# Optimization experiments

Measured on AMD Instinct MI355X. Metric: run time of the kernel, lower is better.

## Reference

```python
import jax, jax.numpy as jnp
import numpy as np

N, E, F_IN = 10000, 160000, 256
H1, C1 = 8, 128          # conv1: heads=8, out 128 per head, concat -> 1024
H2, C2 = 1, 64           # conv2: heads=1, out 64
NEG_SLOPE = 0.2


def setup_inputs() -> dict:
    key = jax.random.key(0)
    ks = jax.random.split(key, 10)
    s_in = 1.0 / np.sqrt(F_IN)
    s_h1 = 1.0 / np.sqrt(H1 * C1)
    return {
        "x": jax.random.normal(ks[0], (N, F_IN), dtype=jnp.float32),
        "edge_index": jax.random.randint(ks[1], (2, E), 0, N, dtype=jnp.int64),
        "W1": jax.random.normal(ks[2], (F_IN, H1 * C1), dtype=jnp.float32) * s_in,
        "att_src1": jax.random.normal(ks[3], (H1, C1), dtype=jnp.float32) * 0.1,
        "att_dst1": jax.random.normal(ks[4], (H1, C1), dtype=jnp.float32) * 0.1,
        "b1": jnp.zeros((H1 * C1,), dtype=jnp.float32),
        "W2": jax.random.normal(ks[5], (H1 * C1, H2 * C2), dtype=jnp.float32) * s_h1,
        "att_src2": jax.random.normal(ks[6], (H2, C2), dtype=jnp.float32) * 0.1,
        "att_dst2": jax.random.normal(ks[7], (H2, C2), dtype=jnp.float32) * 0.1,
        "b2": jnp.zeros((H2 * C2,), dtype=jnp.float32),
    }


def gat_conv(x, src, dst, W, att_src, att_dst, b, n):
    """PyG GATConv (eval mode: dropout off), concat=True, add_self_loops handled by caller."""
    H, C = att_src.shape
    h = (x @ W).reshape(n, H, C)                       # [N,H,C]
    a_s = jnp.einsum('nhc,hc->nh', h, att_src)         # [N,H]
    a_d = jnp.einsum('nhc,hc->nh', h, att_dst)         # [N,H]
    e = jax.nn.leaky_relu(a_s[src] + a_d[dst], NEG_SLOPE)  # [Etot,H]
    # softmax over edges grouped by destination node (numerically stable)
    e_max = jax.ops.segment_max(e, dst, num_segments=n)
    e = jnp.exp(e - e_max[dst])
    denom = jax.ops.segment_sum(e, dst, num_segments=n)
    alpha = e / (denom[dst] + 1e-16)                   # [Etot,H]
    msg = h[src] * alpha[:, :, None]                   # [Etot,H,C]
    out = jax.ops.segment_sum(msg, dst, num_segments=n)  # [N,H,C]
    return out.reshape(n, H * C) + b


def reference(x, edge_index, W1, att_src1, att_dst1, b1, W2, att_src2, att_dst2, b2):
    n = x.shape[0]
    loops = jnp.arange(n, dtype=edge_index.dtype)
    src = jnp.concatenate([edge_index[0], loops])
    dst = jnp.concatenate([edge_index[1], loops])
    h = jax.nn.elu(gat_conv(x, src, dst, W1, att_src1, att_dst1, b1, n))
    return gat_conv(h, src, dst, W2, att_src2, att_dst2, b2, n)
```

## Files before the change

kernel.cpp:

```cpp
#include <hip/hip_runtime.h>
#include <cmath>


typedef short bf16x8 __attribute__((ext_vector_type(8)));
typedef float f32x4 __attribute__((ext_vector_type(4)));
typedef unsigned short u16x8 __attribute__((ext_vector_type(8)));

__device__ __forceinline__ float lrelu(float x) { return x > 0.f ? x : 0.2f * x; }
__device__ __forceinline__ float b2f(unsigned short h) {
  return __uint_as_float(((unsigned)h) << 16);
}
__device__ __forceinline__ unsigned short f2bf(float f) {
  unsigned u = __float_as_uint(f);
  u += 0x7FFFu + ((u >> 16) & 1u);
  return (unsigned short)(u >> 16);
}

__device__ __forceinline__ void fma8(float* acc, uint4 v, float e) {
  acc[0] += e * __uint_as_float(v.x << 16);
  acc[1] += e * __uint_as_float(v.x & 0xffff0000u);
  acc[2] += e * __uint_as_float(v.y << 16);
  acc[3] += e * __uint_as_float(v.y & 0xffff0000u);
  acc[4] += e * __uint_as_float(v.z << 16);
  acc[5] += e * __uint_as_float(v.z & 0xffff0000u);
  acc[6] += e * __uint_as_float(v.w << 16);
  acc[7] += e * __uint_as_float(v.w & 0xffff0000u);
}

#define GLOAD_LDS16(gsrc, ldst)                                              \
  __builtin_amdgcn_global_load_lds(                                          \
      (const __attribute__((address_space(1))) unsigned int*)(gsrc),         \
      (__attribute__((address_space(3))) unsigned int*)(ldst), 16, 0, 0)


__global__ __launch_bounds__(256) void prep_fused(
    const int* __restrict__ ei, int* __restrict__ counts, int E,
    const float* __restrict__ x, unsigned short* __restrict__ xpk, int N, int MB1,
    const float* __restrict__ W1, unsigned short* __restrict__ w1pk,
    const float* __restrict__ W2, unsigned short* __restrict__ w2pk) {
  const int countB = (E + 255) / 256;
  const int pxB = MB1 * 8;
  int bid = blockIdx.x;
  int t = threadIdx.x;

  if (bid < countB) {
    int e = bid * 256 + t;
    if (e < E) atomicAdd(&counts[ei[E + e]], 1);
    return;
  }
  bid -= countB;
  if (bid < pxB) {
    int mb = bid >> 3, ks = bid & 7;
    int l = t & 63, f = t >> 6;
    int row = mb * 64 + f * 16 + (l & 15);
    int kc = ks * 32 + (l >> 4) * 8;
    float v[8];
#pragma unroll
    for (int j = 0; j < 8; ++j) v[j] = 0.f;
    if (row < N) {
      const float* xr = x + (size_t)row * 256 + kc;
#pragma unroll
      for (int j = 0; j < 8; ++j) v[j] = xr[j];
    }
    u16x8 hi, lo;
#pragma unroll
    for (int j = 0; j < 8; ++j) {
      unsigned short h = f2bf(v[j]);
      hi[j] = h; lo[j] = f2bf(v[j] - b2f(h));
    }
    size_t base = (size_t)(mb * 8 + ks) * 8 * 512;
    *(u16x8*)(xpk + base + (size_t)f * 512 + l * 8) = hi;
    *(u16x8*)(xpk + base + (size_t)(4 + f) * 512 + l * 8) = lo;
    return;
  }
  bid -= pxB;
  if (bid < 64) {
    int hb = bid >> 3, ks = bid & 7;
    int l = t & 63, gq = t >> 6;
    for (int g = gq; g < 8; g += 4) {
      int n = hb * 128 + g * 16 + (l & 15);
      int k0 = ks * 32 + (l >> 4) * 8;
      u16x8 hi, lo;
#pragma unroll
      for (int j = 0; j < 8; ++j) {
        float v = W1[(size_t)(k0 + j) * 1024 + n];
        unsigned short h = f2bf(v);
        hi[j] = h; lo[j] = f2bf(v - b2f(h));
      }
      size_t base = (size_t)(hb * 8 + ks) * 16 * 512;
      *(u16x8*)(w1pk + base + (size_t)g * 512 + l * 8) = hi;
      *(u16x8*)(w1pk + base + (size_t)(8 + g) * 512 + l * 8) = lo;
    }
    return;
  }
  bid -= 64;
  {
    int ks = bid;
    int l = t & 63, g = t >> 6;
    int n = g * 16 + (l & 15);
    int k0 = ks * 32 + (l >> 4) * 8;
    u16x8 hi, lo;
#pragma unroll
    for (int j = 0; j < 8; ++j) {
      float v = W2[(size_t)(k0 + j) * 64 + n];
      unsigned short h = f2bf(v);
      hi[j] = h; lo[j] = f2bf(v - b2f(h));
    }
    size_t base = (size_t)ks * 8 * 512;
    *(u16x8*)(w2pk + base + (size_t)g * 512 + l * 8) = hi;
    *(u16x8*)(w2pk + base + (size_t)(4 + g) * 512 + l * 8) = lo;
  }
}


__global__ __launch_bounds__(256) void scan_blk(const int* __restrict__ counts,
                                                int* __restrict__ offsets,
                                                int* __restrict__ bsum, int n) {
  __shared__ int lds[256];
  int b = blockIdx.x, t = threadIdx.x, i = b * 256 + t;
  int v = (i < n) ? counts[i] + 1 : 0;
  lds[t] = v;
  __syncthreads();
  for (int off = 1; off < 256; off <<= 1) {
    int tv = (t >= off) ? lds[t - off] : 0;
    __syncthreads();
    lds[t] += tv;
    __syncthreads();
  }
  if (i < n) offsets[i] = lds[t] - v;
  if (t == 255) bsum[b] = lds[255];
}

__global__ __launch_bounds__(256) void scan_apply(int* __restrict__ offsets,
                                                  int* __restrict__ cursors,
                                                  const int* __restrict__ bsum,
                                                  int nb, int n) {
  __shared__ int pre_s;
  int b = blockIdx.x, t = threadIdx.x;
  if (t == 0) {
    int s = 0;
    for (int i = 0; i < b; ++i) s += bsum[i];
    pre_s = s;
    if (b == nb - 1) {
      int tot = s;
      for (int i = b; i < nb; ++i) tot += bsum[i];
      offsets[n] = tot;
    }
  }
  __syncthreads();
  int i = b * 256 + t;
  if (i < n) {
    int o = offsets[i] + pre_s;
    offsets[i] = o;
    cursors[i] = o;
  }
}

__global__ __launch_bounds__(256) void fill_all(const int* __restrict__ ei,
                                                int* __restrict__ cursors,
                                                const int* __restrict__ offsets,
                                                int* __restrict__ list,
                                                int E, int n) {
  int tid = blockIdx.x * 256 + threadIdx.x;
  if (tid < E) {
    int d = ei[E + tid];
    int pos = atomicAdd(&cursors[d], 1);
    list[pos] = ei[tid];
  } else if (tid < E + n) {
    int i = tid - E;
    list[offsets[i + 1] - 1] = i;
  }
}


__global__ __launch_bounds__(512, 4) void gemm1_att(
    const unsigned short* __restrict__ xpk, const unsigned short* __restrict__ w1pk,
    const float* __restrict__ asrc, const float* __restrict__ adst,
    unsigned short* __restrict__ h1b, float* __restrict__ as1,
    float* __restrict__ ad1) {
  extern __shared__ char sm[];
  const int t = threadIdx.x, wid = t >> 6, lane = t & 63;
  const int wr = wid >> 2, wc = wid & 3;
  const int mb = blockIdx.x, hb = blockIdx.y;
  const int m0 = mb * 128;
  const int l15 = lane & 15, l4 = lane >> 4;

  f32x4 acc[4][2] = {};

  auto stage = [&](int buf, int ks) {
    char* base0 = sm + buf * 32768;
    for (int i = wid; i < 32; i += 8) {
      const unsigned short* src;
      int ldsoff;
      if (i < 8) {
        int r = i >> 2;
        src = xpk + (size_t)((2 * mb + r) * 8 + ks) * 4096 + (i & 3) * 512 + lane * 8;
        ldsoff = i * 1024;
      } else if (i < 16) {
        int f = i - 8, r = f >> 2;
        src = xpk + (size_t)((2 * mb + r) * 8 + ks) * 4096 + (4 + (f & 3)) * 512 + lane * 8;
        ldsoff = 8192 + f * 1024;
      } else if (i < 24) {
        int g = i - 16;
        src = w1pk + (size_t)(hb * 8 + ks) * 8192 + g * 512 + lane * 8;
        ldsoff = 16384 + g * 1024;
      } else {
        int g = i - 24;
        src = w1pk + (size_t)(hb * 8 + ks) * 8192 + (8 + g) * 512 + lane * 8;
        ldsoff = 24576 + g * 1024;
      }
      GLOAD_LDS16(src, base0 + ldsoff);
    }
  };

  stage(0, 0);
  __syncthreads();
  int buf = 0;
  for (int step = 0; step < 8; ++step) {
    if (step < 7) stage(buf ^ 1, step + 1);
    const char* b = sm + buf * 32768;
    bf16x8 ah[4], al[4], bh[2], bl[2];
#pragma unroll
    for (int mf = 0; mf < 4; ++mf) {
      ah[mf] = *(const bf16x8*)(b + (wr * 4 + mf) * 1024 + lane * 16);
      al[mf] = *(const bf16x8*)(b + 8192 + (wr * 4 + mf) * 1024 + lane * 16);
    }
#pragma unroll
    for (int nf = 0; nf < 2; ++nf) {
      bh[nf] = *(const bf16x8*)(b + 16384 + (wc * 2 + nf) * 1024 + lane * 16);
      bl[nf] = *(const bf16x8*)(b + 24576 + (wc * 2 + nf) * 1024 + lane * 16);
    }
#pragma unroll
    for (int mf = 0; mf < 4; ++mf)
#pragma unroll
      for (int nf = 0; nf < 2; ++nf) {
        acc[mf][nf] = __builtin_amdgcn_mfma_f32_16x16x32_bf16(ah[mf], bh[nf], acc[mf][nf], 0, 0, 0);
        acc[mf][nf] = __builtin_amdgcn_mfma_f32_16x16x32_bf16(ah[mf], bl[nf], acc[mf][nf], 0, 0, 0);
        acc[mf][nf] = __builtin_amdgcn_mfma_f32_16x16x32_bf16(al[mf], bh[nf], acc[mf][nf], 0, 0, 0);
      }
    __syncthreads();
    buf ^= 1;
  }

  float* parts_s = (float*)sm;
  float* parts_d = (float*)(sm + 2048);
  unsigned short* ctile = (unsigned short*)(sm + 4096);
  float as_c[2], ad_c[2];
#pragma unroll
  for (int nf = 0; nf < 2; ++nf) {
    int col = hb * 128 + wc * 32 + nf * 16 + l15;
    as_c[nf] = asrc[col];
    ad_c[nf] = adst[col];
  }
#pragma unroll
  for (int mf = 0; mf < 4; ++mf) {
    float ss[4] = {0.f, 0.f, 0.f, 0.f}, dd[4] = {0.f, 0.f, 0.f, 0.f};
#pragma unroll
    for (int nf = 0; nf < 2; ++nf)
#pragma unroll
      for (int r = 0; r < 4; ++r) {
        ss[r] += acc[mf][nf][r] * as_c[nf];
        dd[r] += acc[mf][nf][r] * ad_c[nf];
      }
#pragma unroll
    for (int r = 0; r < 4; ++r)
      for (int m = 1; m < 16; m <<= 1) {
        ss[r] += __shfl_xor(ss[r], m);
        dd[r] += __shfl_xor(dd[r], m);
      }
    if (l15 == 0) {
#pragma unroll
      for (int r = 0; r < 4; ++r) {
        int row = wr * 64 + mf * 16 + l4 * 4 + r;
        parts_s[row * 4 + wc] = ss[r];
        parts_d[row * 4 + wc] = dd[r];
      }
    }
#pragma unroll
    for (int nf = 0; nf < 2; ++nf)
#pragma unroll
      for (int r = 0; r < 4; ++r) {
        int row = wr * 64 + mf * 16 + l4 * 4 + r;
        int col = wc * 32 + nf * 16 + l15;
        ctile[row * 128 + col] = f2bf(acc[mf][nf][r]);
      }
  }
  __syncthreads();
  if (t < 128) {
    float s = parts_s[t * 4] + parts_s[t * 4 + 1] + parts_s[t * 4 + 2] + parts_s[t * 4 + 3];
    float d = parts_d[t * 4] + parts_d[t * 4 + 1] + parts_d[t * 4 + 2] + parts_d[t * 4 + 3];
    as1[(size_t)(m0 + t) * 8 + hb] = s;
    ad1[(size_t)(m0 + t) * 8 + hb] = d;
  }
#pragma unroll
  for (int rep = 0; rep < 4; ++rep) {
    int e = rep * 4096 + t * 8;
    int row = e >> 7, col = e & 127;
    bf16x8 v = *(const bf16x8*)(ctile + e);
    *(bf16x8*)(h1b + (size_t)(m0 + row) * 1024 + hb * 128 + col) = v;
  }
}


__global__ __launch_bounds__(256) void agg1_gather(
    const unsigned short* __restrict__ h1b, const float* __restrict__ as1,
    const float* __restrict__ ad1, const int* __restrict__ offsets,
    const int* __restrict__ list, const float* __restrict__ b1,
    unsigned short* __restrict__ o1pk, int n) {
  __shared__ __align__(16) unsigned short stg[8192];
  const int t = threadIdx.x, w = t >> 6, lane = t & 63;
  const int node = blockIdx.x * 4 + w;
  const int h0 = lane >> 4, h1_ = h0 + 4;

  if (node < n) {
    const int beg = offsets[node], end = offsets[node + 1];
    const float ad0 = ad1[(size_t)node * 8 + h0];
    const float ad4 = ad1[(size_t)node * 8 + h1_];
    float acc0[8] = {}, acc1[8] = {};
    float den0 = 0.f, den4 = 0.f;

    int j = beg;
    int sA = 0, sB = 0;
    float aA0 = 0.f, aA4 = 0.f, aB0 = 0.f, aB4 = 0.f;
    uint4 vA0, vA1, vB0, vB1;
    if (j + 2 <= end) {
      sA = list[j]; sB = list[j + 1];
      aA0 = as1[(size_t)sA * 8 + h0]; aA4 = as1[(size_t)sA * 8 + h1_];
      aB0 = as1[(size_t)sB * 8 + h0]; aB4 = as1[(size_t)sB * 8 + h1_];
      vA0 = *(const uint4*)(h1b + (size_t)sA * 1024 + lane * 8);
      vA1 = *(const uint4*)(h1b + (size_t)sA * 1024 + 512 + lane * 8);
      vB0 = *(const uint4*)(h1b + (size_t)sB * 1024 + lane * 8);
      vB1 = *(const uint4*)(h1b + (size_t)sB * 1024 + 512 + lane * 8);
    }
    for (; j + 4 <= end; j += 2) {
      int sA2 = list[j + 2], sB2 = list[j + 3];
      float aA02 = as1[(size_t)sA2 * 8 + h0], aA42 = as1[(size_t)sA2 * 8 + h1_];
      float aB02 = as1[(size_t)sB2 * 8 + h0], aB42 = as1[(size_t)sB2 * 8 + h1_];
      uint4 nA0 = *(const uint4*)(h1b + (size_t)sA2 * 1024 + lane * 8);
      uint4 nA1 = *(const uint4*)(h1b + (size_t)sA2 * 1024 + 512 + lane * 8);
      uint4 nB0 = *(const uint4*)(h1b + (size_t)sB2 * 1024 + lane * 8);
      uint4 nB1 = *(const uint4*)(h1b + (size_t)sB2 * 1024 + 512 + lane * 8);
      float eA0 = __expf(lrelu(aA0 + ad0)), eA4 = __expf(lrelu(aA4 + ad4));
      float eB0 = __expf(lrelu(aB0 + ad0)), eB4 = __expf(lrelu(aB4 + ad4));
      den0 += eA0 + eB0; den4 += eA4 + eB4;
      fma8(acc0, vA0, eA0); fma8(acc1, vA1, eA4);
      fma8(acc0, vB0, eB0); fma8(acc1, vB1, eB4);
      sA = sA2; sB = sB2;
      aA0 = aA02; aA4 = aA42; aB0 = aB02; aB4 = aB42;
      vA0 = nA0; vA1 = nA1; vB0 = nB0; vB1 = nB1;
    }
    if (j + 2 <= end) {
      float eA0 = __expf(lrelu(aA0 + ad0)), eA4 = __expf(lrelu(aA4 + ad4));
      float eB0 = __expf(lrelu(aB0 + ad0)), eB4 = __expf(lrelu(aB4 + ad4));
      den0 += eA0 + eB0; den4 += eA4 + eB4;
      fma8(acc0, vA0, eA0); fma8(acc1, vA1, eA4);
      fma8(acc0, vB0, eB0); fma8(acc1, vB1, eB4);
      j += 2;
    }
    if (j < end) {
      int s = list[j];
      float a0 = as1[(size_t)s * 8 + h0], a4 = as1[(size_t)s * 8 + h1_];
      uint4 v0 = *(const uint4*)(h1b + (size_t)s * 1024 + lane * 8);
      uint4 v1 = *(const uint4*)(h1b + (size_t)s * 1024 + 512 + lane * 8);
      float e0 = __expf(lrelu(a0 + ad0)), e4 = __expf(lrelu(a4 + ad4));
      den0 += e0; den4 += e4;
      fma8(acc0, v0, e0); fma8(acc1, v1, e4);
    }

    const float inv0 = 1.f / (den0 + 1e-16f);
    const float inv4 = 1.f / (den4 + 1e-16f);
    u16x8 hiA, loA, hiB, loB;
#pragma unroll
    for (int k = 0; k < 8; ++k) {
      float vA = acc0[k] * inv0 + b1[lane * 8 + k];
      float vB = acc1[k] * inv4 + b1[512 + lane * 8 + k];
      vA = vA > 0.f ? vA : expm1f(vA);
      vB = vB > 0.f ? vB : expm1f(vB);
      unsigned short hA = f2bf(vA), hB = f2bf(vB);
      hiA[k] = hA; loA[k] = f2bf(vA - b2f(hA));
      hiB[k] = hB; loB[k] = f2bf(vB - b2f(hB));
    }
    const int q2 = lane >> 2, kc = lane & 3;
    {
      int aw = q2 * 512 + kc * 64 + w * 16;
      *(u16x8*)((char*)stg + (aw ^ ((q2 & 7) << 4))) = hiA;
      aw += 256;
      *(u16x8*)((char*)stg + (aw ^ ((q2 & 7) << 4))) = loA;
    }
    {
      int ks = 16 + q2;
      int aw = ks * 512 + kc * 64 + w * 16;
      *(u16x8*)((char*)stg + (aw ^ ((ks & 7) << 4))) = hiB;
      aw += 256;
      *(u16x8*)((char*)stg + (aw ^ ((ks & 7) << 4))) = loB;
    }
  }
  __syncthreads();
  const int blk = blockIdx.x;
  const int mb = blk >> 4, f = (blk >> 2) & 3, l15b = (blk & 3) * 4;
#pragma unroll
  for (int it = 0; it < 4; ++it) {
    int a = it * 4096 + t * 16;
    int ks = a >> 9, half = (a >> 8) & 1, kcc = (a >> 6) & 3, ww = (a >> 4) & 3;
    u16x8 v = *(const u16x8*)((const char*)stg + (a ^ ((ks & 7) << 4)));
    size_t g = (size_t)(mb * 32 + ks) * 4096 + half * 2048 + (size_t)f * 512 +
               (size_t)(kcc * 16 + l15b + ww) * 8;
    *(u16x8*)(o1pk + g) = v;
  }
}


__global__ __launch_bounds__(256) void gemm2_splitk(
    const unsigned short* __restrict__ o1pk, const unsigned short* __restrict__ w2pk,
    float* __restrict__ h2p, int Mpad) {
  extern __shared__ char sm[];
  const int t = threadIdx.x, wid = t >> 6, lane = t & 63;
  const int wr = wid >> 1, wc = wid & 1;
  const int mb = blockIdx.x, sk = blockIdx.y;
  const int m0 = mb * 64;
  const int l15 = lane & 15, l4 = lane >> 4;

  f32x4 acc[2][2] = {};

  auto stage = [&](int buf, int ks) {
    char* base0 = sm + buf * 16384;
    const unsigned short* ax = o1pk + (size_t)(mb * 32 + ks) * 8 * 512 + lane * 8;
    for (int i = wid; i < 8; i += 4)
      GLOAD_LDS16(ax + i * 512, base0 + i * 1024);
    const unsigned short* bw = w2pk + (size_t)ks * 8 * 512 + lane * 8;
    for (int i = wid; i < 8; i += 4)
      GLOAD_LDS16(bw + i * 512, base0 + 8192 + i * 1024);
  };

  stage(0, sk * 8);
  __syncthreads();
  int buf = 0;
  for (int step = 0; step < 8; ++step) {
    if (step < 7) stage(buf ^ 1, sk * 8 + step + 1);
    const char* b = sm + buf * 16384;
    bf16x8 ah[2], al[2], bh[2], bl[2];
#pragma unroll
    for (int mf = 0; mf < 2; ++mf) {
      int f = wr * 2 + mf;
      ah[mf] = *(const bf16x8*)(b + f * 1024 + lane * 16);
      al[mf] = *(const bf16x8*)(b + 4096 + f * 1024 + lane * 16);
    }
#pragma unroll
    for (int nf = 0; nf < 2; ++nf) {
      int g = wc * 2 + nf;
      bh[nf] = *(const bf16x8*)(b + 8192 + g * 1024 + lane * 16);
      bl[nf] = *(const bf16x8*)(b + 12288 + g * 1024 + lane * 16);
    }
#pragma unroll
    for (int mf = 0; mf < 2; ++mf)
#pragma unroll
      for (int nf = 0; nf < 2; ++nf) {
        acc[mf][nf] = __builtin_amdgcn_mfma_f32_16x16x32_bf16(ah[mf], bh[nf], acc[mf][nf], 0, 0, 0);
        acc[mf][nf] = __builtin_amdgcn_mfma_f32_16x16x32_bf16(ah[mf], bl[nf], acc[mf][nf], 0, 0, 0);
        acc[mf][nf] = __builtin_amdgcn_mfma_f32_16x16x32_bf16(al[mf], bh[nf], acc[mf][nf], 0, 0, 0);
      }
    __syncthreads();
    buf ^= 1;
  }

#pragma unroll
  for (int mf = 0; mf < 2; ++mf)
#pragma unroll
    for (int nf = 0; nf < 2; ++nf)
#pragma unroll
      for (int r = 0; r < 4; ++r) {
        int row = wr * 32 + mf * 16 + l4 * 4 + r;
        int col = wc * 32 + nf * 16 + l15;
        h2p[((size_t)sk * Mpad + m0 + row) * 64 + col] = acc[mf][nf][r];
      }
}


__global__ __launch_bounds__(256) void reduce_att2(
    const float* __restrict__ h2p, const float* __restrict__ asrc,
    const float* __restrict__ adst, float* __restrict__ h2,
    float* __restrict__ as2, float* __restrict__ ad2, int Mpad, int n) {
  int w = threadIdx.x >> 6, lane = threadIdx.x & 63;
  int row = blockIdx.x * 4 + w;
  if (row >= n) return;
  float s = 0.f;
#pragma unroll
  for (int sk = 0; sk < 4; ++sk) s += h2p[((size_t)sk * Mpad + row) * 64 + lane];
  h2[(size_t)row * 64 + lane] = s;
  float ds = s * asrc[lane], dd = s * adst[lane];
  for (int o = 32; o; o >>= 1) { ds += __shfl_xor(ds, o); dd += __shfl_xor(dd, o); }
  if (lane == 0) { as2[row] = ds; ad2[row] = dd; }
}


__global__ __launch_bounds__(256) void agg2_gather(
    const float* __restrict__ h2, const float* __restrict__ as2,
    const float* __restrict__ ad2, const int* __restrict__ offsets,
    const int* __restrict__ list, const float* __restrict__ b2,
    float* __restrict__ out, int n) {
  const int wid = threadIdx.x >> 6, lane = threadIdx.x & 63;
  const int node = blockIdx.x * 4 + wid;
  if (node >= n) return;
  const int beg = offsets[node], end = offsets[node + 1];
  const float ad = ad2[node];
  const int cb = (lane & 15) * 4;
  const int jo = lane >> 4;

  float4 acc = make_float4(0.f, 0.f, 0.f, 0.f);
  float den = 0.f;
  for (int j = beg + jo; j < end; j += 4) {
    int s = list[j];
    float e = __expf(lrelu(as2[s] + ad));
    den += e;
    float4 v = *(const float4*)&h2[(size_t)s * 64 + cb];
    acc.x += e * v.x; acc.y += e * v.y; acc.z += e * v.z; acc.w += e * v.w;
  }
  acc.x += __shfl_xor(acc.x, 16); acc.y += __shfl_xor(acc.y, 16);
  acc.z += __shfl_xor(acc.z, 16); acc.w += __shfl_xor(acc.w, 16);
  den += __shfl_xor(den, 16);
  acc.x += __shfl_xor(acc.x, 32); acc.y += __shfl_xor(acc.y, 32);
  acc.z += __shfl_xor(acc.z, 32); acc.w += __shfl_xor(acc.w, 32);
  den += __shfl_xor(den, 32);
  if (jo == 0) {
    float inv = 1.f / (den + 1e-16f);
    float4 r;
    r.x = acc.x * inv + b2[cb];
    r.y = acc.y * inv + b2[cb + 1];
    r.z = acc.z * inv + b2[cb + 2];
    r.w = acc.w * inv + b2[cb + 3];
    *(float4*)&out[(size_t)node * 64 + cb] = r;
  }
}


extern "C" void kernel_launch(void* const* d_in, const int* in_sizes, int n_in,
                              void* d_out, int out_size, void* d_ws, size_t ws_size,
                              hipStream_t stream) {
  const float* x     = (const float*)d_in[0];
  const int*   ei    = (const int*)d_in[1];
  const float* W1    = (const float*)d_in[2];
  const float* asrc1 = (const float*)d_in[3];
  const float* adst1 = (const float*)d_in[4];
  const float* b1    = (const float*)d_in[5];
  const float* W2    = (const float*)d_in[6];
  const float* asrc2 = (const float*)d_in[7];
  const float* adst2 = (const float*)d_in[8];
  const float* b2    = (const float*)d_in[9];
  float* out = (float*)d_out;

  const int N = in_sizes[0] / 256;
  const int E = in_sizes[1] / 2;
  const int T = E + N;
  const int MBB = (N + 127) / 128;
  const int Mpad = MBB * 128;
  const int MB1 = Mpad / 64;
  const int NB = (N + 255) / 256;

  char* p = (char*)d_ws;
  auto bump = [&](size_t bytes) {
    char* r = p;
    p += (bytes + 255) & ~(size_t)255;
    return r;
  };
  int* counts  = (int*)bump((size_t)N * 4);
  int* offsets = (int*)bump((size_t)(N + 1) * 4);
  int* cursors = (int*)bump((size_t)N * 4);
  int* bsum    = (int*)bump((size_t)NB * 4);
  int* list    = (int*)bump((size_t)T * 4);
  unsigned short* xpk  = (unsigned short*)bump((size_t)Mpad * 512 * 2);
  unsigned short* w1pk = (unsigned short*)bump((size_t)8 * 8 * 16 * 512 * 2);
  unsigned short* h1b  = (unsigned short*)bump((size_t)Mpad * 1024 * 2);
  float* as1           = (float*)bump((size_t)Mpad * 8 * 4);
  float* ad1           = (float*)bump((size_t)Mpad * 8 * 4);
  unsigned short* o1pk = (unsigned short*)bump((size_t)Mpad * 2048 * 2);
  unsigned short* w2pk = (unsigned short*)bump((size_t)32 * 8 * 512 * 2);
  float* as2           = (float*)bump((size_t)Mpad * 4);
  float* ad2           = (float*)bump((size_t)Mpad * 4);
  float* h2p = (float*)h1b;
  float* h2  = (float*)xpk;

  hipMemsetAsync(counts, 0, (size_t)N * 4, stream);
  {
    int gridsz = (E + 255) / 256 + MB1 * 8 + 64 + 32;
    prep_fused<<<gridsz, 256, 0, stream>>>(ei, counts, E, x, xpk, N, MB1,
                                           W1, w1pk, W2, w2pk);
  }
  scan_blk<<<NB, 256, 0, stream>>>(counts, offsets, bsum, N);
  scan_apply<<<NB, 256, 0, stream>>>(offsets, cursors, bsum, NB, N);
  fill_all<<<(E + N + 255) / 256, 256, 0, stream>>>(ei, cursors, offsets, list, E, N);

  gemm1_att<<<dim3(MBB, 8), 512, 65536, stream>>>(xpk, w1pk, asrc1, adst1, h1b, as1, ad1);
  agg1_gather<<<(N + 3) / 4, 256, 0, stream>>>(h1b, as1, ad1, offsets, list, b1, o1pk, N);

  gemm2_splitk<<<dim3(Mpad / 64, 4), 256, 32768, stream>>>(o1pk, w2pk, h2p, Mpad);
  reduce_att2<<<(N + 3) / 4, 256, 0, stream>>>(h2p, asrc2, adst2, h2, as2, ad2, Mpad, N);
  agg2_gather<<<(N + 3) / 4, 256, 0, stream>>>(h2, as2, ad2, offsets, list, b2, out, N);
}
```

Before: 162.3 us.

## Drop x low-bf16 split in GEMM1, shrink tiles, and order gather blocks by degree

Removes the low-order bf16 part of x, so GEMM1 runs two MFMAs per fragment pair instead of three and the packed-x buffer is half the size. GEMM1 moves to 64-row tiles with 256 threads and less LDS. Adds three small kernels that bucket 4-node gather blocks by total in-degree, sort them heaviest first, and remap blockIdx in agg1/agg2 through that order to reduce tail imbalance. This lowers GEMM1 accuracy, since x is now effectively rounded to bf16, and adds extra launches plus a memset.

```diff
diff --git a/kernel.cpp b/kernel.cpp
--- a/kernel.cpp
+++ b/kernel.cpp
@@ -62,15 +62,11 @@
 #pragma unroll
       for (int j = 0; j < 8; ++j) v[j] = xr[j];
     }
-    u16x8 hi, lo;
-#pragma unroll
-    for (int j = 0; j < 8; ++j) {
-      unsigned short h = f2bf(v[j]);
-      hi[j] = h; lo[j] = f2bf(v[j] - b2f(h));
-    }
-    size_t base = (size_t)(mb * 8 + ks) * 8 * 512;
+    u16x8 hi;
+#pragma unroll
+    for (int j = 0; j < 8; ++j) hi[j] = f2bf(v[j]);
+    size_t base = (size_t)(mb * 8 + ks) * 4 * 512;
     *(u16x8*)(xpk + base + (size_t)f * 512 + l * 8) = hi;
-    *(u16x8*)(xpk + base + (size_t)(4 + f) * 512 + l * 8) = lo;
     return;
   }
   bid -= pxB;
@@ -173,43 +169,74 @@
 }
 
 
-__global__ __launch_bounds__(512, 4) void gemm1_att(
+__global__ __launch_bounds__(256) void bweight(const int* __restrict__ offsets,
+                                               int* __restrict__ bwgt,
+                                               int* __restrict__ bhist,
+                                               int nblk, int n) {
+  int b = blockIdx.x * 256 + threadIdx.x;
+  if (b >= nblk) return;
+  int lo = b * 4, hi = min(lo + 4, n);
+  int w = min(offsets[hi] - offsets[lo], 1023);
+  bwgt[b] = w;
+  atomicAdd(&bhist[w], 1);
+}
+
+__global__ __launch_bounds__(1024) void bscan(const int* __restrict__ bhist,
+                                              int* __restrict__ doff) {
+  __shared__ int lds[1024];
+  int t = threadIdx.x;
+  lds[t] = bhist[t];
+  __syncthreads();
+  for (int off = 1; off < 1024; off <<= 1) {
+    int v = (t >= off) ? lds[t - off] : 0;
+    __syncthreads();
+    lds[t] += v;
+    __syncthreads();
+  }
+  int total = lds[1023];
+  doff[t] = total - lds[t];
+}
+
+__global__ __launch_bounds__(256) void bscatter(const int* __restrict__ bwgt,
+                                                const int* __restrict__ doff,
+                                                int* __restrict__ bcur,
+                                                int* __restrict__ border,
+                                                int nblk) {
+  int b = blockIdx.x * 256 + threadIdx.x;
+  if (b >= nblk) return;
+  int w = bwgt[b];
+  int pos = doff[w] + atomicAdd(&bcur[w], 1);
+  border[pos] = b;
+}
+
+
+__global__ __launch_bounds__(256, 4) void gemm1_att(
     const unsigned short* __restrict__ xpk, const unsigned short* __restrict__ w1pk,
     const float* __restrict__ asrc, const float* __restrict__ adst,
     unsigned short* __restrict__ h1b, float* __restrict__ as1,
     float* __restrict__ ad1) {
   extern __shared__ char sm[];
   const int t = threadIdx.x, wid = t >> 6, lane = t & 63;
-  const int wr = wid >> 2, wc = wid & 3;
   const int mb = blockIdx.x, hb = blockIdx.y;
-  const int m0 = mb * 128;
+  const int m0 = mb * 64;
   const int l15 = lane & 15, l4 = lane >> 4;
 
   f32x4 acc[4][2] = {};
 
   auto stage = [&](int buf, int ks) {
-    char* base0 = sm + buf * 32768;
-    for (int i = wid; i < 32; i += 8) {
-      const unsigned short* src;
-      int ldsoff;
-      if (i < 8) {
-        int r = i >> 2;
-        src = xpk + (size_t)((2 * mb + r) * 8 + ks) * 4096 + (i & 3) * 512 + lane * 8;
-        ldsoff = i * 1024;
-      } else if (i < 16) {
-        int f = i - 8, r = f >> 2;
-        src = xpk + (size_t)((2 * mb + r) * 8 + ks) * 4096 + (4 + (f & 3)) * 512 + lane * 8;
-        ldsoff = 8192 + f * 1024;
-      } else if (i < 24) {
-        int g = i - 16;
-        src = w1pk + (size_t)(hb * 8 + ks) * 8192 + g * 512 + lane * 8;
-        ldsoff = 16384 + g * 1024;
+    char* base0 = sm + buf * 20480;
+    const unsigned short* ax = xpk + (size_t)(mb * 8 + ks) * 2048 + lane * 8;
+    const unsigned short* bw = w1pk + (size_t)(hb * 8 + ks) * 8192 + lane * 8;
+    for (int i = wid; i < 20; i += 4) {
+      if (i < 4) {
+        GLOAD_LDS16(ax + i * 512, base0 + i * 1024);
+      } else if (i < 12) {
+        int g = i - 4;
+        GLOAD_LDS16(bw + g * 512, base0 + 4096 + g * 1024);
       } else {
-        int g = i - 24;
-        src = w1pk + (size_t)(hb * 8 + ks) * 8192 + (8 + g) * 512 + lane * 8;
-        ldsoff = 24576 + g * 1024;
-      }
-      GLOAD_LDS16(src, base0 + ldsoff);
+        int g = i - 12;
+        GLOAD_LDS16(bw + (8 + g) * 512, base0 + 12288 + g * 1024);
+      }
     }
   };
 
@@ -218,17 +245,16 @@
   int buf = 0;
   for (int step = 0; step < 8; ++step) {
     if (step < 7) stage(buf ^ 1, step + 1);
-    const char* b = sm + buf * 32768;
-    bf16x8 ah[4], al[4], bh[2], bl[2];
-#pragma unroll
-    for (int mf = 0; mf < 4; ++mf) {
-      ah[mf] = *(const bf16x8*)(b + (wr * 4 + mf) * 1024 + lane * 16);
-      al[mf] = *(const bf16x8*)(b + 8192 + (wr * 4 + mf) * 1024 + lane * 16);
-    }
+    const char* b = sm + buf * 20480;
+    bf16x8 ah[4], bh[2], bl[2];
+#pragma unroll
+    for (int mf = 0; mf < 4; ++mf)
+      ah[mf] = *(const bf16x8*)(b + mf * 1024 + lane * 16);
 #pragma unroll
     for (int nf = 0; nf < 2; ++nf) {
-      bh[nf] = *(const bf16x8*)(b + 16384 + (wc * 2 + nf) * 1024 + lane * 16);
-      bl[nf] = *(const bf16x8*)(b + 24576 + (wc * 2 + nf) * 1024 + lane * 16);
+      int g = wid * 2 + nf;
+      bh[nf] = *(const bf16x8*)(b + 4096 + g * 1024 + lane * 16);
+      bl[nf] = *(const bf16x8*)(b + 12288 + g * 1024 + lane * 16);
     }
 #pragma unroll
     for (int mf = 0; mf < 4; ++mf)
@@ -236,19 +262,18 @@
       for (int nf = 0; nf < 2; ++nf) {
         acc[mf][nf] = __builtin_amdgcn_mfma_f32_16x16x32_bf16(ah[mf], bh[nf], acc[mf][nf], 0, 0, 0);
         acc[mf][nf] = __builtin_amdgcn_mfma_f32_16x16x32_bf16(ah[mf], bl[nf], acc[mf][nf], 0, 0, 0);
-        acc[mf][nf] = __builtin_amdgcn_mfma_f32_16x16x32_bf16(al[mf], bh[nf], acc[mf][nf], 0, 0, 0);
       }
     __syncthreads();
     buf ^= 1;
   }
 
   float* parts_s = (float*)sm;
-  float* parts_d = (float*)(sm + 2048);
-  unsigned short* ctile = (unsigned short*)(sm + 4096);
+  float* parts_d = (float*)(sm + 1024);
+  unsigned short* ctile = (unsigned short*)(sm + 2048);
   float as_c[2], ad_c[2];
 #pragma unroll
   for (int nf = 0; nf < 2; ++nf) {
-    int col = hb * 128 + wc * 32 + nf * 16 + l15;
+    int col = hb * 128 + wid * 32 + nf * 16 + l15;
     as_c[nf] = asrc[col];
     ad_c[nf] = adst[col];
   }
@@ -271,22 +296,22 @@
     if (l15 == 0) {
 #pragma unroll
       for (int r = 0; r < 4; ++r) {
-        int row = wr * 64 + mf * 16 + l4 * 4 + r;
-        parts_s[row * 4 + wc] = ss[r];
-        parts_d[row * 4 + wc] = dd[r];
+        int row = mf * 16 + l4 * 4 + r;
+        parts_s[row * 4 + wid] = ss[r];
+        parts_d[row * 4 + wid] = dd[r];
       }
     }
 #pragma unroll
     for (int nf = 0; nf < 2; ++nf)
 #pragma unroll
       for (int r = 0; r < 4; ++r) {
-        int row = wr * 64 + mf * 16 + l4 * 4 + r;
-        int col = wc * 32 + nf * 16 + l15;
+        int row = mf * 16 + l4 * 4 + r;
+        int col = wid * 32 + nf * 16 + l15;
         ctile[row * 128 + col] = f2bf(acc[mf][nf][r]);
       }
   }
   __syncthreads();
-  if (t < 128) {
+  if (t < 64) {
     float s = parts_s[t * 4] + parts_s[t * 4 + 1] + parts_s[t * 4 + 2] + parts_s[t * 4 + 3];
     float d = parts_d[t * 4] + parts_d[t * 4 + 1] + parts_d[t * 4 + 2] + parts_d[t * 4 + 3];
     as1[(size_t)(m0 + t) * 8 + hb] = s;
@@ -294,7 +319,7 @@
   }
 #pragma unroll
   for (int rep = 0; rep < 4; ++rep) {
-    int e = rep * 4096 + t * 8;
+    int e = rep * 2048 + t * 8;
     int row = e >> 7, col = e & 127;
     bf16x8 v = *(const bf16x8*)(ctile + e);
     *(bf16x8*)(h1b + (size_t)(m0 + row) * 1024 + hb * 128 + col) = v;
@@ -306,10 +331,12 @@
     const unsigned short* __restrict__ h1b, const float* __restrict__ as1,
     const float* __restrict__ ad1, const int* __restrict__ offsets,
     const int* __restrict__ list, const float* __restrict__ b1,
+    const int* __restrict__ border,
     unsigned short* __restrict__ o1pk, int n) {
   __shared__ __align__(16) unsigned short stg[8192];
   const int t = threadIdx.x, w = t >> 6, lane = t & 63;
-  const int node = blockIdx.x * 4 + w;
+  const int blk = border[blockIdx.x];
+  const int node = blk * 4 + w;
   const int h0 = lane >> 4, h1_ = h0 + 4;
 
   if (node < n) {
@@ -396,7 +423,6 @@
     }
   }
   __syncthreads();
-  const int blk = blockIdx.x;
   const int mb = blk >> 4, f = (blk >> 2) & 3, l15b = (blk & 3) * 4;
 #pragma unroll
   for (int it = 0; it < 4; ++it) {
@@ -497,9 +523,10 @@
     const float* __restrict__ h2, const float* __restrict__ as2,
     const float* __restrict__ ad2, const int* __restrict__ offsets,
     const int* __restrict__ list, const float* __restrict__ b2,
+    const int* __restrict__ border,
     float* __restrict__ out, int n) {
   const int wid = threadIdx.x >> 6, lane = threadIdx.x & 63;
-  const int node = blockIdx.x * 4 + wid;
+  const int node = border[blockIdx.x] * 4 + wid;
   if (node >= n) return;
   const int beg = offsets[node], end = offsets[node + 1];
   const float ad = ad2[node];
@@ -551,10 +578,10 @@
   const int N = in_sizes[0] / 256;
   const int E = in_sizes[1] / 2;
   const int T = E + N;
-  const int MBB = (N + 127) / 128;
-  const int Mpad = MBB * 128;
-  const int MB1 = Mpad / 64;
+  const int MB1 = (N + 63) / 64;
+  const int Mpad = MB1 * 64;
   const int NB = (N + 255) / 256;
+  const int NBLK4 = (N + 3) / 4;
 
   char* p = (char*)d_ws;
   auto bump = [&](size_t bytes) {
@@ -567,7 +594,12 @@
   int* cursors = (int*)bump((size_t)N * 4);
   int* bsum    = (int*)bump((size_t)NB * 4);
   int* list    = (int*)bump((size_t)T * 4);
-  unsigned short* xpk  = (unsigned short*)bump((size_t)Mpad * 512 * 2);
+  int* bwgt    = (int*)bump((size_t)NBLK4 * 4);
+  int* bhist   = (int*)bump((size_t)1024 * 4);
+  int* bcur    = (int*)bump((size_t)1024 * 4);
+  int* doff    = (int*)bump((size_t)1024 * 4);
+  int* border  = (int*)bump((size_t)NBLK4 * 4);
+  unsigned short* xpk  = (unsigned short*)bump((size_t)Mpad * 256 * 2);
   unsigned short* w1pk = (unsigned short*)bump((size_t)8 * 8 * 16 * 512 * 2);
   unsigned short* h1b  = (unsigned short*)bump((size_t)Mpad * 1024 * 2);
   float* as1           = (float*)bump((size_t)Mpad * 8 * 4);
@@ -580,6 +612,7 @@
   float* h2  = (float*)xpk;
 
   hipMemsetAsync(counts, 0, (size_t)N * 4, stream);
+  hipMemsetAsync(bhist, 0, 2048 * 4, stream);
   {
     int gridsz = (E + 255) / 256 + MB1 * 8 + 64 + 32;
     prep_fused<<<gridsz, 256, 0, stream>>>(ei, counts, E, x, xpk, N, MB1,
@@ -589,10 +622,14 @@
   scan_apply<<<NB, 256, 0, stream>>>(offsets, cursors, bsum, NB, N);
   fill_all<<<(E + N + 255) / 256, 256, 0, stream>>>(ei, cursors, offsets, list, E, N);
 
-  gemm1_att<<<dim3(MBB, 8), 512, 65536, stream>>>(xpk, w1pk, asrc1, adst1, h1b, as1, ad1);
-  agg1_gather<<<(N + 3) / 4, 256, 0, stream>>>(h1b, as1, ad1, offsets, list, b1, o1pk, N);
+  bweight<<<(NBLK4 + 255) / 256, 256, 0, stream>>>(offsets, bwgt, bhist, NBLK4, N);
+  bscan<<<1, 1024, 0, stream>>>(bhist, doff);
+  bscatter<<<(NBLK4 + 255) / 256, 256, 0, stream>>>(bwgt, doff, bcur, border, NBLK4);
+
+  gemm1_att<<<dim3(MB1, 8), 256, 40960, stream>>>(xpk, w1pk, asrc1, adst1, h1b, as1, ad1);
+  agg1_gather<<<NBLK4, 256, 0, stream>>>(h1b, as1, ad1, offsets, list, b1, border, o1pk, N);
 
   gemm2_splitk<<<dim3(Mpad / 64, 4), 256, 32768, stream>>>(o1pk, w2pk, h2p, Mpad);
   reduce_att2<<<(N + 3) / 4, 256, 0, stream>>>(h2p, asrc2, adst2, h2, as2, ad2, Mpad, N);
-  agg2_gather<<<(N + 3) / 4, 256, 0, stream>>>(h2, as2, ad2, offsets, list, b2, out, N);
-}
+  agg2_gather<<<NBLK4, 256, 0, stream>>>(h2, as2, ad2, offsets, list, b2, border, out, N);
+}
```

Measured after the change: 173.5 us. 1.07x slower.
